# Kernel tuning notes

Hardware: AMD Instinct MI355X
Metric: run time of the kernel (lower is better)

## Reference

```python
import jax, jax.numpy as jnp
import numpy as np
import math

IN_DIM = 768
FREQ = IN_DIM // 2 + 1          # 385
K = max(1, int(FREQ * 0.1))     # 38
MLP_IN = 2 * K                  # 76
HID = 256
LN_EPS = 1e-5


def _spectral_mask(task_id=0):
    # Faithful port of PiNoiseBiLoRA._get_spectral_mask
    avail = np.arange(1, FREQ)
    mt = 20
    idx = avail[task_id % mt::mt]
    if len(idx) >= K:
        idx = idx[:K]
    else:
        needed = K - len(idx)
        rf = math.ceil(needed / len(idx))
        idx = np.concatenate([idx, np.tile(idx, rf)[:needed]])
    return idx.astype(np.int32)


def setup_inputs() -> dict:
    key = jax.random.key(0)
    ks = jax.random.split(key, 6)
    B, S = 8, 4096
    x = jax.random.normal(ks[0], (B, S, IN_DIM), dtype=jnp.float32)
    eps = jax.random.normal(ks[1], (B, S, MLP_IN), dtype=jnp.float32)
    indices = jnp.asarray(_spectral_mask(0))
    w_scale = 0.05
    mu_w1 = jax.random.normal(ks[2], (HID, MLP_IN), dtype=jnp.float32) * w_scale
    mu_w2 = jax.random.normal(ks[3], (MLP_IN, HID), dtype=jnp.float32) * w_scale
    sg_w1 = jax.random.normal(ks[4], (HID, MLP_IN), dtype=jnp.float32) * w_scale
    sg_w2 = jax.random.normal(ks[5], (MLP_IN, HID), dtype=jnp.float32) * w_scale
    zeros_h = jnp.zeros((HID,), jnp.float32)
    zeros_o = jnp.zeros((MLP_IN,), jnp.float32)
    ones_h = jnp.ones((HID,), jnp.float32)
    return {
        'x': x, 'eps': eps, 'indices': indices,
        'mu_w1': mu_w1, 'mu_b1': zeros_h, 'mu_g': ones_h, 'mu_beta': zeros_h,
        'mu_w2': mu_w2, 'mu_b2': zeros_o,
        'sg_w1': sg_w1, 'sg_b1': zeros_h, 'sg_g': ones_h, 'sg_beta': zeros_h,
        'sg_w2': sg_w2, 'sg_b2': zeros_o,
    }


def _mlp(x, w1, b1, g, beta, w2, b2):
    # Linear -> LayerNorm -> GELU(exact) -> Linear
    h = x @ w1.T + b1
    mu = h.mean(axis=-1, keepdims=True)
    var = jnp.mean((h - mu) ** 2, axis=-1, keepdims=True)
    h = (h - mu) * jax.lax.rsqrt(var + LN_EPS) * g + beta
    h = jax.nn.gelu(h, approximate=False)
    return h @ w2.T + b2


def reference(x, eps, indices,
              mu_w1, mu_b1, mu_g, mu_beta, mu_w2, mu_b2,
              sg_w1, sg_b1, sg_g, sg_beta, sg_w2, sg_b2):
    # Training-mode forward of PiNoiseBiLoRA
    x_freq = jnp.fft.rfft(x, axis=-1)            # [B,S,FREQ] complex64
    x_sel = x_freq[..., indices]                 # gather k freq bins
    x_in = jnp.concatenate([x_sel.real, x_sel.imag], axis=-1)  # [B,S,2k]
    mu = _mlp(x_in, mu_w1, mu_b1, mu_g, mu_beta, mu_w2, mu_b2)
    sigma = _mlp(x_in, sg_w1, sg_b1, sg_g, sg_beta, sg_w2, sg_b2)
    z = mu + eps * sigma                         # reparameterization
    z_complex = jax.lax.complex(z[..., :K], z[..., K:]).astype(jnp.complex64)
    noise = jnp.zeros(x_freq.shape, jnp.complex64).at[..., indices].add(z_complex)
    return jnp.fft.irfft(noise, n=IN_DIM, axis=-1)
```

## Files before the change

kernel.cpp:

```cpp
#include <hip/hip_runtime.h>
#include <hip/hip_bf16.h>
#include <math.h>

#define INDIM 768
#define NROWS 32768
#define KSEL  38
#define NCOLS 76
#define HID   256
#define LN_EPS 1e-5f

typedef float  f32x4  __attribute__((ext_vector_type(4)));
typedef __bf16 bf16x8 __attribute__((ext_vector_type(8)));

#define MFMA16(a,b,c) __builtin_amdgcn_mfma_f32_16x16x32_bf16((a),(b),(c),0,0,0)

#define OFF_BFP 0
#define OFF_W1P 122880
#define OFF_W2P 221184
#define OFF_BSP 303104

__global__ void k_prep(const int* __restrict__ idxs,
                       const float* __restrict__ mu_w1, const float* __restrict__ sg_w1,
                       const float* __restrict__ mu_w2, const float* __restrict__ sg_w2,
                       __bf16* __restrict__ BfP, __bf16* __restrict__ W1P,
                       __bf16* __restrict__ W2P, __bf16* __restrict__ BsP)
{
    int tid = blockIdx.x * blockDim.x + threadIdx.x;
    int nth = gridDim.x * blockDim.x;
    const float TH = 6.28318530717958647692f / (float)INDIM;

    for (int e = tid; e < 120 * 512; e += nth) {
        int frag = e >> 9, lane = (e >> 3) & 63, j = e & 7;
        int kc = frag / 5, nt = frag % 5;
        int c = nt * 16 + (lane & 15);
        int k = kc * 32 + ((lane >> 4) << 3) + j;
        float v = 0.f;
        if (c < NCOLS) {
            int cc = (c < KSEL) ? c : c - KSEL;
            int f = idxs[cc];
            int m = (f * k) % INDIM;
            float s, co; sincosf(TH * (float)m, &s, &co);
            v = (c < KSEL) ? co : -s;
        }
        BfP[e] = (__bf16)v;
    }
    for (int e = tid; e < 96 * 512; e += nth) {
        int frag = e >> 9, lane = (e >> 3) & 63, j = e & 7;
        int mlp = frag / 48; int r = frag % 48;
        int nt = r / 3, ks = r % 3;
        int row = nt * 16 + (lane & 15);
        int k = ks * 32 + ((lane >> 4) << 3) + j;
        const float* W = mlp ? sg_w1 : mu_w1;
        W1P[e] = (__bf16)((k < NCOLS) ? W[row * NCOLS + k] : 0.f);
    }
    for (int e = tid; e < 80 * 512; e += nth) {
        int frag = e >> 9, lane = (e >> 3) & 63, j = e & 7;
        int mlp = frag / 40; int r = frag % 40;
        int nt = r / 8, ks = r % 8;
        int row = nt * 16 + (lane & 15);
        int k = ks * 32 + ((lane >> 4) << 3) + j;
        const float* W = mlp ? sg_w2 : mu_w2;
        W2P[e] = (__bf16)((row < NCOLS) ? W[row * HID + k] : 0.f);
    }
    for (int e = tid; e < 144 * 512; e += nth) {
        int frag = e >> 9, lane = (e >> 3) & 63, j = e & 7;
        int nt = frag / 3, ks = frag % 3;
        int n = nt * 16 + (lane & 15);
        int k = ks * 32 + ((lane >> 4) << 3) + j;
        float v = 0.f;
        if (k < NCOLS) {
            int cc = (k < KSEL) ? k : k - KSEL;
            int f = idxs[cc];
            int m = (f * n) % INDIM;
            float s, co; sincosf(TH * (float)m, &s, &co);
            v = ((k < KSEL) ? co : -s) * (2.0f / (float)INDIM);
        }
        BsP[e] = (__bf16)v;
    }
}

static __device__ inline float gelu_fast(float v) {
    float u = v * (0.79788456080286535588f + 0.03567740813636141f * v * v);
    return v / (1.f + __expf(-2.f * u));
}

__global__ __launch_bounds__(256, 2) void k_fused(
    const float* __restrict__ x, const float* __restrict__ eps,
    const __bf16* __restrict__ BfG, const __bf16* __restrict__ W1G,
    const __bf16* __restrict__ W2G, const __bf16* __restrict__ BsG,
    const float* __restrict__ mu_b1, const float* __restrict__ mu_g,
    const float* __restrict__ mu_be, const float* __restrict__ mu_b2,
    const float* __restrict__ sg_b1, const float* __restrict__ sg_g,
    const float* __restrict__ sg_be, const float* __restrict__ sg_b2,
    float* __restrict__ out)
{
    __shared__ __bf16 sstage[24576];
    __shared__ __bf16 stb[4][1664];
    int tid = threadIdx.x;
    int w = tid >> 6, lane = tid & 63, q = lane >> 4, l16 = lane & 15;
    int rbase = blockIdx.x * 64 + w * 16;
    __bf16* tb = stb[w];

    auto stage = [&](const __bf16* src, int n16) {
        for (int i = tid; i < n16; i += 256)
            *(bf16x8*)&sstage[i * 8] = *(const bf16x8*)&src[i * 8];
    };

    f32x4 acc[5] = {};
    {
        const float* xrow = x + (size_t)(rbase + l16) * INDIM + q * 8;
        for (int c = 0; c < 3; ++c) {
            stage(BfG + (size_t)c * 40 * 512, 2560);
            __syncthreads();
            #pragma unroll
            for (int kk = 0; kk < 8; ++kk) {
                int kc = c * 8 + kk;
                float4 f0 = ((const float4*)(xrow + kc * 32))[0];
                float4 f1 = ((const float4*)(xrow + kc * 32))[1];
                union { __bf16 h[8]; bf16x8 v; } a;
                a.h[0]=(__bf16)f0.x; a.h[1]=(__bf16)f0.y; a.h[2]=(__bf16)f0.z; a.h[3]=(__bf16)f0.w;
                a.h[4]=(__bf16)f1.x; a.h[5]=(__bf16)f1.y; a.h[6]=(__bf16)f1.z; a.h[7]=(__bf16)f1.w;
                #pragma unroll
                for (int nt = 0; nt < 5; ++nt) {
                    bf16x8 b = *(const bf16x8*)&sstage[(kk * 5 + nt) * 512 + lane * 8];
                    acc[nt] = MFMA16(a.v, b, acc[nt]);
                }
            }
            __syncthreads();
        }
    }
    #pragma unroll
    for (int nt = 0; nt < 5; ++nt)
        #pragma unroll
        for (int r = 0; r < 4; ++r)
            tb[(q * 4 + r) * 104 + nt * 16 + l16] = (__bf16)acc[nt][r];
    #pragma unroll
    for (int r = 0; r < 4; ++r)
        tb[(q * 4 + r) * 104 + 80 + l16] = (__bf16)0.f;
    bf16x8 a1[3];
    #pragma unroll
    for (int ks = 0; ks < 3; ++ks)
        a1[ks] = *(const bf16x8*)&tb[l16 * 104 + ks * 32 + q * 8];

    f32x4 o2[2][5];
    #pragma unroll
    for (int mlp = 0; mlp < 2; ++mlp) {
        const float* b1 = mlp ? sg_b1 : mu_b1;
        const float* g  = mlp ? sg_g  : mu_g;
        const float* be = mlp ? sg_be : mu_be;

        stage(W1G + (size_t)mlp * 48 * 512, 3072);
        __syncthreads();
        f32x4 h[16] = {};
        #pragma unroll
        for (int nt = 0; nt < 16; ++nt)
            #pragma unroll
            for (int ks = 0; ks < 3; ++ks) {
                bf16x8 b = *(const bf16x8*)&sstage[(nt * 3 + ks) * 512 + lane * 8];
                h[nt] = MFMA16(a1[ks], b, h[nt]);
            }
        __syncthreads();

        float s[4] = {}, ss[4] = {};
        #pragma unroll
        for (int nt = 0; nt < 16; ++nt) {
            float bb = b1[nt * 16 + l16];
            #pragma unroll
            for (int r = 0; r < 4; ++r) {
                float v = h[nt][r] + bb; h[nt][r] = v;
                s[r] += v; ss[r] += v * v;
            }
        }
        #pragma unroll
        for (int off = 1; off < 16; off <<= 1)
            #pragma unroll
            for (int r = 0; r < 4; ++r) {
                s[r] += __shfl_xor(s[r], off); ss[r] += __shfl_xor(ss[r], off);
            }
        float mean[4], rstd[4];
        #pragma unroll
        for (int r = 0; r < 4; ++r) {
            mean[r] = s[r] * (1.f / 256.f);
            rstd[r] = rsqrtf(ss[r] * (1.f / 256.f) - mean[r] * mean[r] + LN_EPS);
        }
        __bf16* gw = &sstage[w * 16 * 264];
        #pragma unroll
        for (int nt = 0; nt < 16; ++nt) {
            int i = nt * 16 + l16;
            float gv = g[i], bev = be[i];
            #pragma unroll
            for (int r = 0; r < 4; ++r)
                gw[(q * 4 + r) * 264 + i] =
                    (__bf16)gelu_fast((h[nt][r] - mean[r]) * rstd[r] * gv + bev);
        }
        bf16x8 a2[8];
        #pragma unroll
        for (int ks = 0; ks < 8; ++ks)
            a2[ks] = *(const bf16x8*)&gw[l16 * 264 + ks * 32 + q * 8];
        __syncthreads();

        stage(W2G + (size_t)mlp * 40 * 512, 2560);
        __syncthreads();
        #pragma unroll
        for (int nt = 0; nt < 5; ++nt) {
            f32x4 oc = {};
            #pragma unroll
            for (int ks = 0; ks < 8; ++ks) {
                bf16x8 b = *(const bf16x8*)&sstage[(nt * 8 + ks) * 512 + lane * 8];
                oc = MFMA16(a2[ks], b, oc);
            }
            o2[mlp][nt] = oc;
        }
        __syncthreads();
    }

    #pragma unroll
    for (int nt = 0; nt < 5; ++nt) {
        int j = nt * 16 + l16;
        float b2m = (j < NCOLS) ? mu_b2[j] : 0.f;
        float b2s = (j < NCOLS) ? sg_b2[j] : 0.f;
        #pragma unroll
        for (int r = 0; r < 4; ++r) {
            float z = 0.f;
            if (j < NCOLS) {
                float e = eps[(size_t)(rbase + q * 4 + r) * NCOLS + j];
                z = (o2[0][nt][r] + b2m) + e * (o2[1][nt][r] + b2s);
            }
            tb[(q * 4 + r) * 104 + j] = (__bf16)z;
        }
    }
    #pragma unroll
    for (int r = 0; r < 4; ++r)
        tb[(q * 4 + r) * 104 + 80 + l16] = (__bf16)0.f;
    bf16x8 az[3];
    #pragma unroll
    for (int ks = 0; ks < 3; ++ks)
        az[ks] = *(const bf16x8*)&tb[l16 * 104 + ks * 32 + q * 8];

    for (int c = 0; c < 3; ++c) {
        stage(BsG + (size_t)c * 48 * 512, 3072);
        __syncthreads();
        #pragma unroll
        for (int ntl = 0; ntl < 16; ++ntl) {
            f32x4 oc = {};
            #pragma unroll
            for (int ks = 0; ks < 3; ++ks) {
                bf16x8 b = *(const bf16x8*)&sstage[(ntl * 3 + ks) * 512 + lane * 8];
                oc = MFMA16(az[ks], b, oc);
            }
            int col = (c * 16 + ntl) * 16 + l16;
            #pragma unroll
            for (int r = 0; r < 4; ++r)
                out[(size_t)(rbase + q * 4 + r) * INDIM + col] = oc[r];
        }
        __syncthreads();
    }
}

extern "C" void kernel_launch(void* const* d_in, const int* in_sizes, int n_in,
                              void* d_out, int out_size, void* d_ws, size_t ws_size,
                              hipStream_t stream)
{
    const float* x     = (const float*)d_in[0];
    const float* eps   = (const float*)d_in[1];
    const int*   idxs  = (const int*)  d_in[2];
    const float* mu_w1 = (const float*)d_in[3];
    const float* mu_b1 = (const float*)d_in[4];
    const float* mu_g  = (const float*)d_in[5];
    const float* mu_be = (const float*)d_in[6];
    const float* mu_w2 = (const float*)d_in[7];
    const float* mu_b2 = (const float*)d_in[8];
    const float* sg_w1 = (const float*)d_in[9];
    const float* sg_b1 = (const float*)d_in[10];
    const float* sg_g  = (const float*)d_in[11];
    const float* sg_be = (const float*)d_in[12];
    const float* sg_w2 = (const float*)d_in[13];
    const float* sg_b2 = (const float*)d_in[14];
    float* out = (float*)d_out;

    char* ws = (char*)d_ws;
    __bf16* BfP = (__bf16*)(ws + OFF_BFP);
    __bf16* W1P = (__bf16*)(ws + OFF_W1P);
    __bf16* W2P = (__bf16*)(ws + OFF_W2P);
    __bf16* BsP = (__bf16*)(ws + OFF_BSP);

    hipLaunchKernelGGL(k_prep, dim3(1024), dim3(256), 0, stream,
                       idxs, mu_w1, sg_w1, mu_w2, sg_w2, BfP, W1P, W2P, BsP);
    hipLaunchKernelGGL(k_fused, dim3(NROWS / 64), dim3(256), 0, stream,
                       x, eps, BfP, W1P, W2P, BsP,
                       mu_b1, mu_g, mu_be, mu_b2,
                       sg_b1, sg_g, sg_be, sg_b2, out);
}
```

Baseline: 249.4 us.

## Split row tiles across wave pairs and read packed weights from global

Each block now handles 32 rows, with two waves per 16-row tile. In the forward DFT the pair splits the K dimension and combines partial sums through shared memory. In the MLP stage one wave computes the mu branch and the other the sigma branch, and the inverse DFT output columns are split between them. The per-stage shared-memory weight staging and its barriers are removed, so B fragments are read directly from global/L2. Shared memory shrinks, allowing a launch bound of 4 blocks per CU, at the cost of more global weight traffic and extra cross-wave reductions.

```diff
diff --git a/kernel.cpp b/kernel.cpp
--- a/kernel.cpp
+++ b/kernel.cpp
@@ -84,176 +84,189 @@
     return v / (1.f + __expf(-2.f * u));
 }
 
-__global__ __launch_bounds__(256, 2) void k_fused(
+__global__ __launch_bounds__(256, 4) void k_fused(
     const float* __restrict__ x, const float* __restrict__ eps,
-    const __bf16* __restrict__ BfG, const __bf16* __restrict__ W1G,
-    const __bf16* __restrict__ W2G, const __bf16* __restrict__ BsG,
+    const __bf16* __restrict__ Bf, const __bf16* __restrict__ W1f,
+    const __bf16* __restrict__ W2f, const __bf16* __restrict__ Bs,
     const float* __restrict__ mu_b1, const float* __restrict__ mu_g,
     const float* __restrict__ mu_be, const float* __restrict__ mu_b2,
     const float* __restrict__ sg_b1, const float* __restrict__ sg_g,
     const float* __restrict__ sg_be, const float* __restrict__ sg_b2,
     float* __restrict__ out)
 {
-    __shared__ __bf16 sstage[24576];
-    __shared__ __bf16 stb[4][1664];
+    __shared__ __bf16 tbuf[2][1664];
+    __shared__ char   ureg[17408];
+    float*  PA = (float*)ureg;
+    __bf16* GW = (__bf16*)ureg;
+
     int tid = threadIdx.x;
     int w = tid >> 6, lane = tid & 63, q = lane >> 4, l16 = lane & 15;
-    int rbase = blockIdx.x * 64 + w * 16;
-    __bf16* tb = stb[w];
-
-    auto stage = [&](const __bf16* src, int n16) {
-        for (int i = tid; i < n16; i += 256)
-            *(bf16x8*)&sstage[i * 8] = *(const bf16x8*)&src[i * 8];
-    };
+    int t = w >> 1, p = w & 1;
+    int rbase = blockIdx.x * 32 + t * 16;
 
     f32x4 acc[5] = {};
     {
-        const float* xrow = x + (size_t)(rbase + l16) * INDIM + q * 8;
-        for (int c = 0; c < 3; ++c) {
-            stage(BfG + (size_t)c * 40 * 512, 2560);
-            __syncthreads();
-            #pragma unroll
-            for (int kk = 0; kk < 8; ++kk) {
-                int kc = c * 8 + kk;
-                float4 f0 = ((const float4*)(xrow + kc * 32))[0];
-                float4 f1 = ((const float4*)(xrow + kc * 32))[1];
-                union { __bf16 h[8]; bf16x8 v; } a;
-                a.h[0]=(__bf16)f0.x; a.h[1]=(__bf16)f0.y; a.h[2]=(__bf16)f0.z; a.h[3]=(__bf16)f0.w;
-                a.h[4]=(__bf16)f1.x; a.h[5]=(__bf16)f1.y; a.h[6]=(__bf16)f1.z; a.h[7]=(__bf16)f1.w;
-                #pragma unroll
-                for (int nt = 0; nt < 5; ++nt) {
-                    bf16x8 b = *(const bf16x8*)&sstage[(kk * 5 + nt) * 512 + lane * 8];
-                    acc[nt] = MFMA16(a.v, b, acc[nt]);
-                }
+        const float* xrow = x + (size_t)(rbase + l16) * INDIM + p * 384 + q * 8;
+        #pragma unroll
+        for (int kk = 0; kk < 12; ++kk) {
+            int kc = p * 12 + kk;
+            float4 f0 = ((const float4*)(xrow + kk * 32))[0];
+            float4 f1 = ((const float4*)(xrow + kk * 32))[1];
+            union { __bf16 h[8]; bf16x8 v; } a;
+            a.h[0]=(__bf16)f0.x; a.h[1]=(__bf16)f0.y; a.h[2]=(__bf16)f0.z; a.h[3]=(__bf16)f0.w;
+            a.h[4]=(__bf16)f1.x; a.h[5]=(__bf16)f1.y; a.h[6]=(__bf16)f1.z; a.h[7]=(__bf16)f1.w;
+            #pragma unroll
+            for (int nt = 0; nt < 5; ++nt) {
+                bf16x8 b = *(const bf16x8*)&Bf[(size_t)((kc * 5 + nt) * 64 + lane) * 8];
+                acc[nt] = MFMA16(a.v, b, acc[nt]);
             }
-            __syncthreads();
-        }
-    }
-    #pragma unroll
-    for (int nt = 0; nt < 5; ++nt)
+        }
+    }
+    if (p == 1) {
+        #pragma unroll
+        for (int nt = 0; nt < 5; ++nt)
+            #pragma unroll
+            for (int r = 0; r < 4; ++r)
+                PA[t * 1280 + (q * 4 + r) * 80 + nt * 16 + l16] = acc[nt][r];
+    }
+    __syncthreads();
+    if (p == 0) {
+        #pragma unroll
+        for (int nt = 0; nt < 5; ++nt)
+            #pragma unroll
+            for (int r = 0; r < 4; ++r) {
+                float v = acc[nt][r] + PA[t * 1280 + (q * 4 + r) * 80 + nt * 16 + l16];
+                tbuf[t][(q * 4 + r) * 104 + nt * 16 + l16] = (__bf16)v;
+            }
         #pragma unroll
         for (int r = 0; r < 4; ++r)
-            tb[(q * 4 + r) * 104 + nt * 16 + l16] = (__bf16)acc[nt][r];
-    #pragma unroll
-    for (int r = 0; r < 4; ++r)
-        tb[(q * 4 + r) * 104 + 80 + l16] = (__bf16)0.f;
+            tbuf[t][(q * 4 + r) * 104 + 80 + l16] = (__bf16)0.f;
+    }
+    __syncthreads();
     bf16x8 a1[3];
     #pragma unroll
     for (int ks = 0; ks < 3; ++ks)
-        a1[ks] = *(const bf16x8*)&tb[l16 * 104 + ks * 32 + q * 8];
-
-    f32x4 o2[2][5];
-    #pragma unroll
-    for (int mlp = 0; mlp < 2; ++mlp) {
-        const float* b1 = mlp ? sg_b1 : mu_b1;
-        const float* g  = mlp ? sg_g  : mu_g;
-        const float* be = mlp ? sg_be : mu_be;
-
-        stage(W1G + (size_t)mlp * 48 * 512, 3072);
-        __syncthreads();
-        f32x4 h[16] = {};
-        #pragma unroll
-        for (int nt = 0; nt < 16; ++nt)
-            #pragma unroll
-            for (int ks = 0; ks < 3; ++ks) {
-                bf16x8 b = *(const bf16x8*)&sstage[(nt * 3 + ks) * 512 + lane * 8];
-                h[nt] = MFMA16(a1[ks], b, h[nt]);
-            }
-        __syncthreads();
-
-        float s[4] = {}, ss[4] = {};
-        #pragma unroll
-        for (int nt = 0; nt < 16; ++nt) {
-            float bb = b1[nt * 16 + l16];
-            #pragma unroll
-            for (int r = 0; r < 4; ++r) {
-                float v = h[nt][r] + bb; h[nt][r] = v;
-                s[r] += v; ss[r] += v * v;
-            }
-        }
-        #pragma unroll
-        for (int off = 1; off < 16; off <<= 1)
-            #pragma unroll
-            for (int r = 0; r < 4; ++r) {
-                s[r] += __shfl_xor(s[r], off); ss[r] += __shfl_xor(ss[r], off);
-            }
-        float mean[4], rstd[4];
+        a1[ks] = *(const bf16x8*)&tbuf[t][l16 * 104 + ks * 32 + q * 8];
+
+    const float* b1 = p ? sg_b1 : mu_b1;
+    const float* g  = p ? sg_g  : mu_g;
+    const float* be = p ? sg_be : mu_be;
+
+    f32x4 h[16] = {};
+    #pragma unroll
+    for (int nt = 0; nt < 16; ++nt)
+        #pragma unroll
+        for (int ks = 0; ks < 3; ++ks) {
+            bf16x8 b = *(const bf16x8*)&W1f[(size_t)((p * 48 + nt * 3 + ks) * 64 + lane) * 8];
+            h[nt] = MFMA16(a1[ks], b, h[nt]);
+        }
+    float s[4] = {}, ss[4] = {};
+    #pragma unroll
+    for (int nt = 0; nt < 16; ++nt) {
+        float bb = b1[nt * 16 + l16];
         #pragma unroll
         for (int r = 0; r < 4; ++r) {
-            mean[r] = s[r] * (1.f / 256.f);
-            rstd[r] = rsqrtf(ss[r] * (1.f / 256.f) - mean[r] * mean[r] + LN_EPS);
-        }
-        __bf16* gw = &sstage[w * 16 * 264];
-        #pragma unroll
-        for (int nt = 0; nt < 16; ++nt) {
+            float v = h[nt][r] + bb; h[nt][r] = v;
+            s[r] += v; ss[r] += v * v;
+        }
+    }
+    #pragma unroll
+    for (int off = 1; off < 16; off <<= 1)
+        #pragma unroll
+        for (int r = 0; r < 4; ++r) {
+            s[r] += __shfl_xor(s[r], off); ss[r] += __shfl_xor(ss[r], off);
+        }
+    float mean[4], rstd[4];
+    #pragma unroll
+    for (int r = 0; r < 4; ++r) {
+        mean[r] = s[r] * (1.f / 256.f);
+        rstd[r] = rsqrtf(ss[r] * (1.f / 256.f) - mean[r] * mean[r] + LN_EPS);
+    }
+    __bf16* gw = &GW[w * 2176];
+    bf16x8 a2[8];
+    #pragma unroll
+    for (int half = 0; half < 2; ++half) {
+        #pragma unroll
+        for (int ntl = 0; ntl < 8; ++ntl) {
+            int nt = half * 8 + ntl;
             int i = nt * 16 + l16;
             float gv = g[i], bev = be[i];
             #pragma unroll
             for (int r = 0; r < 4; ++r)
-                gw[(q * 4 + r) * 264 + i] =
+                gw[(q * 4 + r) * 136 + ntl * 16 + l16] =
                     (__bf16)gelu_fast((h[nt][r] - mean[r]) * rstd[r] * gv + bev);
         }
-        bf16x8 a2[8];
-        #pragma unroll
-        for (int ks = 0; ks < 8; ++ks)
-            a2[ks] = *(const bf16x8*)&gw[l16 * 264 + ks * 32 + q * 8];
-        __syncthreads();
-
-        stage(W2G + (size_t)mlp * 40 * 512, 2560);
-        __syncthreads();
+        #pragma unroll
+        for (int ks = 0; ks < 4; ++ks)
+            a2[half * 4 + ks] = *(const bf16x8*)&gw[l16 * 136 + ks * 32 + q * 8];
+    }
+
+    f32x4 o[5] = {};
+    #pragma unroll
+    for (int nt = 0; nt < 5; ++nt)
+        #pragma unroll
+        for (int ks = 0; ks < 8; ++ks) {
+            bf16x8 b = *(const bf16x8*)&W2f[(size_t)((p * 40 + nt * 8 + ks) * 64 + lane) * 8];
+            o[nt] = MFMA16(a2[ks], b, o[nt]);
+        }
+
+    __syncthreads();
+    float ev[5][4];
+    if (p == 0) {
+        #pragma unroll
+        for (int nt = 0; nt < 5; ++nt)
+            #pragma unroll
+            for (int r = 0; r < 4; ++r)
+                PA[t * 1280 + (q * 4 + r) * 80 + nt * 16 + l16] = o[nt][r];
+    } else {
         #pragma unroll
         for (int nt = 0; nt < 5; ++nt) {
-            f32x4 oc = {};
-            #pragma unroll
-            for (int ks = 0; ks < 8; ++ks) {
-                bf16x8 b = *(const bf16x8*)&sstage[(nt * 8 + ks) * 512 + lane * 8];
-                oc = MFMA16(a2[ks], b, oc);
+            int j = nt * 16 + l16;
+            #pragma unroll
+            for (int r = 0; r < 4; ++r)
+                ev[nt][r] = (j < NCOLS)
+                    ? eps[(size_t)(rbase + q * 4 + r) * NCOLS + j] : 0.f;
+        }
+    }
+    __syncthreads();
+    if (p == 1) {
+        #pragma unroll
+        for (int nt = 0; nt < 5; ++nt) {
+            int j = nt * 16 + l16;
+            float b2m = (j < NCOLS) ? mu_b2[j] : 0.f;
+            float b2s = (j < NCOLS) ? sg_b2[j] : 0.f;
+            #pragma unroll
+            for (int r = 0; r < 4; ++r) {
+                float z = 0.f;
+                if (j < NCOLS) {
+                    float omu = PA[t * 1280 + (q * 4 + r) * 80 + j];
+                    z = (omu + b2m) + ev[nt][r] * (o[nt][r] + b2s);
+                }
+                tbuf[t][(q * 4 + r) * 104 + j] = (__bf16)z;
             }
-            o2[mlp][nt] = oc;
-        }
-        __syncthreads();
-    }
-
-    #pragma unroll
-    for (int nt = 0; nt < 5; ++nt) {
-        int j = nt * 16 + l16;
-        float b2m = (j < NCOLS) ? mu_b2[j] : 0.f;
-        float b2s = (j < NCOLS) ? sg_b2[j] : 0.f;
-        #pragma unroll
-        for (int r = 0; r < 4; ++r) {
-            float z = 0.f;
-            if (j < NCOLS) {
-                float e = eps[(size_t)(rbase + q * 4 + r) * NCOLS + j];
-                z = (o2[0][nt][r] + b2m) + e * (o2[1][nt][r] + b2s);
-            }
-            tb[(q * 4 + r) * 104 + j] = (__bf16)z;
-        }
-    }
-    #pragma unroll
-    for (int r = 0; r < 4; ++r)
-        tb[(q * 4 + r) * 104 + 80 + l16] = (__bf16)0.f;
+        }
+        #pragma unroll
+        for (int r = 0; r < 4; ++r)
+            tbuf[t][(q * 4 + r) * 104 + 80 + l16] = (__bf16)0.f;
+    }
+    __syncthreads();
     bf16x8 az[3];
     #pragma unroll
     for (int ks = 0; ks < 3; ++ks)
-        az[ks] = *(const bf16x8*)&tb[l16 * 104 + ks * 32 + q * 8];
-
-    for (int c = 0; c < 3; ++c) {
-        stage(BsG + (size_t)c * 48 * 512, 3072);
-        __syncthreads();
-        #pragma unroll
-        for (int ntl = 0; ntl < 16; ++ntl) {
-            f32x4 oc = {};
-            #pragma unroll
-            for (int ks = 0; ks < 3; ++ks) {
-                bf16x8 b = *(const bf16x8*)&sstage[(ntl * 3 + ks) * 512 + lane * 8];
-                oc = MFMA16(az[ks], b, oc);
-            }
-            int col = (c * 16 + ntl) * 16 + l16;
-            #pragma unroll
-            for (int r = 0; r < 4; ++r)
-                out[(size_t)(rbase + q * 4 + r) * INDIM + col] = oc[r];
-        }
-        __syncthreads();
+        az[ks] = *(const bf16x8*)&tbuf[t][l16 * 104 + ks * 32 + q * 8];
+
+    #pragma unroll 6
+    for (int k = 0; k < 24; ++k) {
+        int nt = p * 24 + k;
+        f32x4 oc = {};
+        #pragma unroll
+        for (int ks = 0; ks < 3; ++ks) {
+            bf16x8 b = *(const bf16x8*)&Bs[(size_t)((nt * 3 + ks) * 64 + lane) * 8];
+            oc = MFMA16(az[ks], b, oc);
+        }
+        #pragma unroll
+        for (int r = 0; r < 4; ++r)
+            out[(size_t)(rbase + q * 4 + r) * INDIM + nt * 16 + l16] = oc[r];
     }
 }
 
@@ -286,7 +299,7 @@
 
     hipLaunchKernelGGL(k_prep, dim3(1024), dim3(256), 0, stream,
                        idxs, mu_w1, sg_w1, mu_w2, sg_w2, BfP, W1P, W2P, BsP);
-    hipLaunchKernelGGL(k_fused, dim3(NROWS / 64), dim3(256), 0, stream,
+    hipLaunchKernelGGL(k_fused, dim3(NROWS / 32), dim3(256), 0, stream,
                        x, eps, BfP, W1P, W2P, BsP,
                        mu_b1, mu_g, mu_be, mu_b2,
                        sg_b1, sg_g, sg_be, sg_b2, out);
```

Measured after the change: 247.7 us. About the same (-0.7%).
